# Kernel tuning notes

Measured on AMD Instinct MI355X. Metric: run time of the kernel, lower is better.

Reference implementation:

```python
import jax, jax.numpy as jnp
import numpy as np

B, S, H, NH, T = 4, 512, 512, 8, 3
DH = H // NH
DTS = H // T  # 170, per-timescale encoder width
EPS = 1e-5

def _ln(x, g, b):
    m = jnp.mean(x, axis=-1, keepdims=True)
    v = jnp.mean((x - m) ** 2, axis=-1, keepdims=True)
    return (x - m) * jax.lax.rsqrt(v + EPS) * g + b

def _gelu(x):
    return jax.nn.gelu(x, approximate=False)

def _mha(x, qkv_W, qkv_b, out_W, out_b, mask):
    # x: [B,S,H]; qkv_W: [H,3H]; mask: [B,S,S] float additive or None
    qkv = x @ qkv_W + qkv_b
    q, k, v = jnp.split(qkv, 3, axis=-1)
    q = q.reshape(B, S, NH, DH)
    k = k.reshape(B, S, NH, DH)
    v = v.reshape(B, S, NH, DH)
    scores = jnp.einsum('bqhd,bkhd->bhqk', q, k) / jnp.sqrt(jnp.float32(DH))
    if mask is not None:
        scores = scores + mask[:, None, :, :]
    attn = jax.nn.softmax(scores, axis=-1)
    o = jnp.einsum('bhqk,bkhd->bqhd', attn, v).reshape(B, S, H)
    return o @ out_W + out_b

def setup_inputs() -> dict:
    key = jax.random.key(0)
    ks = jax.random.split(key, 32)
    r = lambda i, shape, s=0.02: (jax.random.normal(ks[i], shape, dtype=jnp.float32) * s)
    inp = {}
    inp['x'] = jax.random.normal(ks[0], (B, S, H), dtype=jnp.float32)
    inp['timestamps'] = jax.random.uniform(ks[1], (B, S), dtype=jnp.float32) * 1e6
    # per-timescale encoders (stacked over T)
    inp['enc_W'] = r(2, (T, 2, DTS), 0.5)
    inp['enc_b'] = jnp.zeros((T, DTS), jnp.float32)
    inp['enc_ln_g'] = jnp.ones((T, DTS), jnp.float32)
    inp['enc_ln_b'] = jnp.zeros((T, DTS), jnp.float32)
    # per-timescale MHA
    inp['qkv_W'] = r(3, (T, H, 3 * H))
    inp['qkv_b'] = jnp.zeros((T, 3 * H), jnp.float32)
    inp['attn_out_W'] = r(4, (T, H, H))
    inp['attn_out_b'] = jnp.zeros((T, H), jnp.float32)
    # time mixer
    inp['mixer_W1'] = r(5, (T * H, H))
    inp['mixer_b1'] = jnp.zeros((H,), jnp.float32)
    inp['mixer_ln_g'] = jnp.ones((H,), jnp.float32)
    inp['mixer_ln_b'] = jnp.zeros((H,), jnp.float32)
    inp['mixer_W2'] = r(6, (H, T))
    inp['mixer_b2'] = jnp.zeros((T,), jnp.float32)
    # transformer encoder layer (post-norm, gelu, ffn=4H)
    inp['el_qkv_W'] = r(7, (H, 3 * H))
    inp['el_qkv_b'] = jnp.zeros((3 * H,), jnp.float32)
    inp['el_out_W'] = r(8, (H, H))
    inp['el_out_b'] = jnp.zeros((H,), jnp.float32)
    inp['el_ln1_g'] = jnp.ones((H,), jnp.float32)
    inp['el_ln1_b'] = jnp.zeros((H,), jnp.float32)
    inp['el_ff_W1'] = r(9, (H, 4 * H))
    inp['el_ff_b1'] = jnp.zeros((4 * H,), jnp.float32)
    inp['el_ff_W2'] = r(10, (4 * H, H))
    inp['el_ff_b2'] = jnp.zeros((H,), jnp.float32)
    inp['el_ln2_g'] = jnp.ones((H,), jnp.float32)
    inp['el_ln2_b'] = jnp.zeros((H,), jnp.float32)
    # output projection
    inp['op_W'] = r(11, (H, H))
    inp['op_b'] = jnp.zeros((H,), jnp.float32)
    inp['op_ln_g'] = jnp.ones((H,), jnp.float32)
    inp['op_ln_b'] = jnp.zeros((H,), jnp.float32)
    return inp

def reference(x, timestamps, enc_W, enc_b, enc_ln_g, enc_ln_b, qkv_W, qkv_b, attn_out_W, attn_out_b,
              mixer_W1, mixer_b1, mixer_ln_g, mixer_ln_b, mixer_W2, mixer_b2,
              el_qkv_W, el_qkv_b, el_out_W, el_out_b, el_ln1_g, el_ln1_b,
              el_ff_W1, el_ff_b1, el_ff_W2, el_ff_b2, el_ln2_g, el_ln2_b,
              op_W, op_b, op_ln_g, op_ln_b):
    # pairwise time features [B,S,S]
    time_diff = timestamps[:, :, None] - timestamps[:, None, :]
    direction = jnp.sign(time_diff)
    magnitude = jnp.log1p(jnp.abs(time_diff) / 3600.0)
    outs = []
    for i in range(T):
        mag = magnitude / (10.0 ** i)
        tf = jnp.stack([direction, mag], axis=-1)            # [B,S,S,2]
        e = tf @ enc_W[i] + enc_b[i]                          # [B,S,S,DTS]
        e = _gelu(_ln(e, enc_ln_g[i], enc_ln_b[i]))
        mask = jnp.mean(e, axis=-1)                           # [B,S,S] additive attn mask
        outs.append(_mha(x, qkv_W[i], qkv_b[i], attn_out_W[i], attn_out_b[i], mask))
    combined = jnp.concatenate(outs, axis=-1)                 # [B,S,T*H]
    m = _gelu(_ln(combined @ mixer_W1 + mixer_b1, mixer_ln_g, mixer_ln_b))
    mix = jax.nn.softmax(m @ mixer_W2 + mixer_b2, axis=-1)    # [B,S,T]
    weighted = sum(mix[..., i:i + 1] * outs[i] for i in range(T))
    # post-norm transformer encoder layer
    sa = _mha(weighted, el_qkv_W, el_qkv_b, el_out_W, el_out_b, None)
    h1 = _ln(weighted + sa, el_ln1_g, el_ln1_b)
    ff = _gelu(h1 @ el_ff_W1 + el_ff_b1) @ el_ff_W2 + el_ff_b2
    h2 = _ln(h1 + ff, el_ln2_g, el_ln2_b)
    out = _ln(h2 @ op_W + op_b, op_ln_g, op_ln_b)
    return out
```

## Files before the change

kernel.cpp:

```cpp
#include <hip/hip_runtime.h>
#include <hip/hip_bf16.h>
#include <math.h>

#define Bq 4
#define Sq 512
#define Hq 512
#define NHq 8
#define Tq 3
#define DTSq 170
#define BSq 2048
#define ENCSTRIDE 520
#define NLUT 2048
#define MAGMAXf 5.6304994f

typedef float f32x4 __attribute__((ext_vector_type(4)));
typedef __bf16 bf16x4 __attribute__((ext_vector_type(4)));
typedef __bf16 bf16x8 __attribute__((ext_vector_type(8)));

__device__ __forceinline__ float gelu_f(float x){
  return 0.5f * x * (1.0f + erff(x * 0.70710678118654752f));
}

__device__ __forceinline__ void gload16(const void* g, void* l){
  __builtin_amdgcn_global_load_lds((const __attribute__((address_space(1))) void*)g,
                                   (__attribute__((address_space(3))) void*)l, 16, 0, 0);
}

__device__ __forceinline__ float waveReduceSum(float v){
  #pragma unroll
  for (int off = 32; off > 0; off >>= 1) v += __shfl_xor(v, off);
  return v;
}

__device__ __forceinline__ float blockReduce(float v, float* red){
  int tid = threadIdx.x;
  __syncthreads();
  red[tid] = v; __syncthreads();
  for (int s = 128; s > 0; s >>= 1){
    if (tid < s) red[tid] += red[tid + s];
    __syncthreads();
  }
  return red[0];
}

__global__ __launch_bounds__(256) void enc_prep(const float* __restrict__ encW,
                                                const float* __restrict__ encB,
                                                float* __restrict__ out){
  int t = blockIdx.x, tid = threadIdx.x;
  __shared__ float red[256];
  const float* W0 = encW + t * 2 * DTSq;
  const float* W1 = W0 + DTSq;
  const float* Bv = encB + t * DTSq;
  float w0 = (tid < DTSq) ? W0[tid] : 0.f;
  float w1 = (tid < DTSq) ? W1[tid] : 0.f;
  float bv = (tid < DTSq) ? Bv[tid] : 0.f;
  const float invD = 1.0f / (float)DTSq;
  float m0 = blockReduce(w0, red) * invD;
  float m1 = blockReduce(w1, red) * invD;
  float mb = blockReduce(bv, red) * invD;
  float c0 = (tid < DTSq) ? (w0 - m0) : 0.f;
  float c1 = (tid < DTSq) ? (w1 - m1) : 0.f;
  float cb = (tid < DTSq) ? (bv - mb) : 0.f;
  float* op = out + t * ENCSTRIDE;
  if (tid < DTSq){
    op[tid] = c0; op[DTSq + tid] = c1; op[2 * DTSq + tid] = cb;
  }
  float pa = blockReduce(c0 * c0, red) * invD;
  float pb = blockReduce(c1 * c1, red) * invD;
  float pc = blockReduce(c0 * c1, red) * invD;
  float pd = blockReduce(c0 * cb, red) * invD;
  float pe = blockReduce(c1 * cb, red) * invD;
  float pf = blockReduce(cb * cb, red) * invD;
  if (tid == 0){
    op[3 * DTSq + 0] = pa; op[3 * DTSq + 1] = pb; op[3 * DTSq + 2] = pc;
    op[3 * DTSq + 3] = pd; op[3 * DTSq + 4] = pe; op[3 * DTSq + 5] = pf;
  }
}

__global__ __launch_bounds__(256) void mask_lut_build(const float* __restrict__ enc,
                                                      const float* __restrict__ g,
                                                      const float* __restrict__ be,
                                                      float* __restrict__ lut){
  int td = blockIdx.x;
  int t = td / 3, dsel = td % 3;
  float d = (float)(dsel - 1);
  __shared__ float sw0[DTSq], sw1[DTSq], sbc[DTSq], sg[DTSq], sbe[DTSq];
  const float* ep = enc + t * ENCSTRIDE;
  for (int c = threadIdx.x; c < DTSq; c += 256){
    sw0[c] = ep[c]; sw1[c] = ep[DTSq + c]; sbc[c] = ep[2 * DTSq + c];
    sg[c] = g[t * DTSq + c]; sbe[c] = be[t * DTSq + c];
  }
  __syncthreads();
  float A  = ep[3 * DTSq + 0], Bs = ep[3 * DTSq + 1], Cs = ep[3 * DTSq + 2];
  float Ds = ep[3 * DTSq + 3], Es = ep[3 * DTSq + 4], Fs = ep[3 * DTSq + 5];
  int e = blockIdx.y * 256 + threadIdx.x;
  float tscale = (t == 0) ? 1.f : ((t == 1) ? 0.1f : 0.01f);
  float m = (MAGMAXf / (float)(NLUT - 1)) * (float)e * tscale;
  float var = fabsf(d) * A + m * m * Bs + Fs + 2.f * (d * m * Cs + d * Ds + m * Es);
  float rs = rsqrtf(var + 1e-5f);
  float sum = 0.f;
  for (int c = 0; c < DTSq; ++c){
    float ee = fmaf(m, sw1[c], fmaf(d, sw0[c], sbc[c]));
    float n = fmaf(ee * rs, sg[c], sbe[c]);
    sum += n * 0.5f * (1.0f + erff(n * 0.70710678118654752f));
  }
  lut[td * NLUT + e] = sum * (1.0f / (float)DTSq);
}

__global__ __launch_bounds__(256) void mask_fill(const float* __restrict__ ts,
                                                 const float* __restrict__ lut,
                                                 __bf16* __restrict__ maskbuf){
  int bi = blockIdx.x;
  int b = bi >> 9, i = bi & 511;
  float tsi = ts[bi];
  for (int j0 = 0; j0 < Sq; j0 += 256){
    int j = j0 + threadIdx.x;
    float dt = tsi - ts[(b << 9) + j];
    int dsel = (dt > 0.f) ? 2 : ((dt < 0.f) ? 0 : 1);
    float mag = log1pf(fabsf(dt) * (1.0f / 3600.0f));
    float u = mag * ((float)(NLUT - 1) / MAGMAXf);
    int i0 = (int)u; if (i0 > NLUT - 2) i0 = NLUT - 2;
    float f = u - (float)i0;
    #pragma unroll
    for (int t = 0; t < Tq; ++t){
      const float* lp = lut + (t * 3 + dsel) * NLUT + i0;
      float v = lp[0] + f * (lp[1] - lp[0]);
      maskbuf[(((size_t)(t * Bq + b) * Sq + i) * Sq) + j] = (__bf16)v;
    }
  }
}

struct CvtEnt { const float* W; __bf16* WT; int ldw, ldt, ntn, start; };
struct CvtArgs { CvtEnt e[12]; };

__global__ __launch_bounds__(256) void cvt_wT_all(CvtArgs a){
  int bid = blockIdx.x;
  int i = 0;
  #pragma unroll
  for (int k = 1; k < 12; ++k) if (bid >= a.e[k].start) i = k;
  const float* W = a.e[i].W;
  __bf16* WT = a.e[i].WT;
  int ldw = a.e[i].ldw, ldt = a.e[i].ldt;
  int local = bid - a.e[i].start;
  int tn = local % a.e[i].ntn, tk = local / a.e[i].ntn;
  int n0 = tn * 64, k0 = tk * 64;
  __shared__ float T[64][65];
  int tid = threadIdx.x;
  #pragma unroll
  for (int q = 0; q < 16; ++q){
    int lin = q * 256 + tid;
    int r = lin >> 6, c = lin & 63;
    T[r][c] = W[(size_t)(k0 + r) * ldw + n0 + c];
  }
  __syncthreads();
  #pragma unroll
  for (int q = 0; q < 16; ++q){
    int lin = q * 256 + tid;
    int n = lin >> 6, k = lin & 63;
    WT[(size_t)(n0 + n) * ldt + k0 + k] = (__bf16)T[k][n];
  }
}

__global__ __launch_bounds__(256) void cvt_bf(const float* __restrict__ in,
                                              __bf16* __restrict__ out, int n){
  int idx = (blockIdx.x * 256 + threadIdx.x) * 4;
  if (idx < n){
    float4 v = *(const float4*)&in[idx];
    bf16x4 r; r[0]=(__bf16)v.x; r[1]=(__bf16)v.y; r[2]=(__bf16)v.z; r[3]=(__bf16)v.w;
    *(bf16x4*)&out[idx] = r;
  }
}

template<int BM>
__global__ __launch_bounds__(256) void gemm_pipe(
    const __bf16* __restrict__ A, int lda, size_t sAz,
    const __bf16* __restrict__ BT, int ldb, size_t sBz,
    const float* __restrict__ bias, int sBiasz,
    float* __restrict__ C32, __bf16* __restrict__ C16, int ldc, size_t sCz,
    int K, int act)
{
  constexpr int MF = BM / 32;
  constexpr int ABYTES = BM * 128;
  constexpr int BBYTES = 64 * 128;
  __shared__ __bf16 lds[(2 * (ABYTES + BBYTES)) / 2];
  int tid = threadIdx.x;

  int gx = gridDim.x, nwg = gx * gridDim.y;
  int lin = blockIdx.x + gx * blockIdx.y;
  int q8 = nwg >> 3;
  int swz = (lin & 7) * q8 + (lin >> 3);
  int bx = swz % gx, by = swz / gx;

  int z = blockIdx.z;
  A  += (size_t)z * sAz;
  BT += (size_t)z * sBz;
  const float* bz = bias ? bias + (size_t)z * sBiasz : nullptr;
  size_t cbase = (size_t)z * sCz;
  int brow = by * BM, bcol = bx * 64;

  int lane = tid & 63, w = tid >> 6;
  int wr = (w >> 1) * (BM / 2), wc = (w & 1) * 32;
  int lr = lane & 15, lg = lane >> 4;

  f32x4 acc[MF][2];
  #pragma unroll
  for (int m = 0; m < MF; ++m)
    #pragma unroll
    for (int n = 0; n < 2; ++n) acc[m][n] = (f32x4){0.f, 0.f, 0.f, 0.f};

  char* lbase = (char*)lds;

  auto stage = [&](int buf, int ko){
    char* ab = lbase + buf * (ABYTES + BBYTES);
    #pragma unroll
    for (int qq = 0; qq < BM / 32; ++qq){
      int byte = (qq * 256 + tid) * 16;
      int row = byte >> 7, col8 = byte & 127;
      int src = col8 ^ ((row & 7) << 4);
      gload16(&A[(size_t)(brow + row) * lda + ko + (src >> 1)], ab + byte);
    }
    char* bb = ab + ABYTES;
    #pragma unroll
    for (int qq = 0; qq < 2; ++qq){
      int byte = (qq * 256 + tid) * 16;
      int row = byte >> 7, col8 = byte & 127;
      int src = col8 ^ ((row & 7) << 4);
      gload16(&BT[(size_t)(bcol + row) * ldb + ko + (src >> 1)], bb + byte);
    }
  };

  stage(0, 0);
  int nk = K >> 6;
  for (int kt = 0; kt < nk; ++kt){
    int cur = kt & 1;
    if (kt + 1 < nk){
      stage(cur ^ 1, (kt + 1) << 6);
      if constexpr (BM == 64) asm volatile("s_waitcnt vmcnt(4)" ::: "memory");
      else                    asm volatile("s_waitcnt vmcnt(6)" ::: "memory");
    } else {
      asm volatile("s_waitcnt vmcnt(0)" ::: "memory");
    }
    __builtin_amdgcn_s_barrier();
    __builtin_amdgcn_sched_barrier(0);
    char* ab = lbase + cur * (ABYTES + BBYTES);
    char* bb = ab + ABYTES;
    #pragma unroll
    for (int s = 0; s < 2; ++s){
      bf16x8 af[MF], bfr[2];
      #pragma unroll
      for (int m = 0; m < MF; ++m){
        int row = wr + m * 16 + lr;
        int col8 = (s * 64 + lg * 16) ^ ((row & 7) << 4);
        af[m] = *(const bf16x8*)(ab + row * 128 + col8);
      }
      #pragma unroll
      for (int n = 0; n < 2; ++n){
        int row = wc + n * 16 + lr;
        int col8 = (s * 64 + lg * 16) ^ ((row & 7) << 4);
        bfr[n] = *(const bf16x8*)(bb + row * 128 + col8);
      }
      #pragma unroll
      for (int m = 0; m < MF; ++m)
        #pragma unroll
        for (int n = 0; n < 2; ++n)
          acc[m][n] = __builtin_amdgcn_mfma_f32_16x16x32_bf16(af[m], bfr[n], acc[m][n], 0, 0, 0);
    }
    asm volatile("" ::: "memory");
    __builtin_amdgcn_s_barrier();
  }

  #pragma unroll
  for (int m = 0; m < MF; ++m){
    #pragma unroll
    for (int n = 0; n < 2; ++n){
      int col = bcol + wc + n * 16 + lr;
      float bv = bz ? bz[col] : 0.f;
      #pragma unroll
      for (int j = 0; j < 4; ++j){
        int row = brow + wr + m * 16 + lg * 4 + j;
        float v = acc[m][n][j] + bv;
        if (act) v = gelu_f(v);
        size_t idx = cbase + (size_t)row * ldc + col;
        if (C32) C32[idx] = v;
        if (C16) C16[idx] = (__bf16)v;
      }
    }
  }
}

template<bool HM>
__global__ __launch_bounds__(256) void flash_attn(
    const __bf16* __restrict__ qkv, size_t sQz,
    const __bf16* __restrict__ vt,  size_t sVz,
    const __bf16* __restrict__ mask, size_t sMz,
    __bf16* __restrict__ ctx, size_t sCz)
{
  int t = blockIdx.z;
  qkv += (size_t)t * sQz;
  vt  += (size_t)t * sVz;
  ctx += (size_t)t * sCz;
  const __bf16* mk = HM ? mask + (size_t)t * sMz : nullptr;

  int lin = blockIdx.x + (blockIdx.y << 3);
  int swz = (lin & 7) * 32 + (lin >> 3);
  int io = (swz & 7) * 64;
  int bh = swz >> 3;
  int b = bh >> 3, h = bh & 7;

  constexpr int KB = 64 * 128;
  __shared__ __bf16 lds[(2 * 2 * KB) / 2];
  __shared__ __bf16 Ps[4][16][72];
  int tid = threadIdx.x, lane = tid & 63, w = tid >> 6;
  int lr = lane & 15, lg = lane >> 4;

  const __bf16* qrow = &qkv[(size_t)(b * Sq + io + w * 16 + lr) * 1536 + h * 64];
  bf16x8 q0 = *(const bf16x8*)&qrow[lg * 8];
  bf16x8 q1 = *(const bf16x8*)&qrow[32 + lg * 8];

  char* lb = (char*)lds;
  auto stage = [&](int buf, int jo){
    char* kb = lb + buf * (2 * KB);
    #pragma unroll
    for (int qq = 0; qq < 2; ++qq){
      int byte = (qq * 256 + tid) * 16;
      int row = byte >> 7, col8 = byte & 127;
      int src = col8 ^ ((row & 7) << 4);
      gload16(&qkv[(size_t)(b * Sq + jo + row) * 1536 + 512 + h * 64 + (src >> 1)], kb + byte);
    }
    char* vb = kb + KB;
    #pragma unroll
    for (int qq = 0; qq < 2; ++qq){
      int byte = (qq * 256 + tid) * 16;
      int row = byte >> 7, col8 = byte & 127;
      int src = col8 ^ ((row & 7) << 4);
      gload16(&vt[((size_t)bh * 64 + row) * Sq + jo + (src >> 1)], vb + byte);
    }
  };

  f32x4 o[4];
  #pragma unroll
  for (int n = 0; n < 4; ++n) o[n] = (f32x4){0.f, 0.f, 0.f, 0.f};
  float mrow[4] = {-1e30f, -1e30f, -1e30f, -1e30f};
  float lrow[4] = {0.f, 0.f, 0.f, 0.f};

  stage(0, 0);
  #pragma unroll
  for (int kt = 0; kt < 8; ++kt){
    int cur = kt & 1;
    int jo = kt << 6;

    float mv[4][4];
    if (HM){
      #pragma unroll
      for (int n = 0; n < 4; ++n)
        #pragma unroll
        for (int reg = 0; reg < 4; ++reg)
          mv[n][reg] = (float)mk[((size_t)(b * Sq + io + w * 16 + lg * 4 + reg)) * Sq + jo + n * 16 + lr];
    }

    if (kt + 1 < 8){
      stage(cur ^ 1, (kt + 1) << 6);
      if (HM) asm volatile("s_waitcnt vmcnt(20)" ::: "memory");
      else    asm volatile("s_waitcnt vmcnt(4)"  ::: "memory");
    } else {
      asm volatile("s_waitcnt vmcnt(0)" ::: "memory");
    }
    __builtin_amdgcn_s_barrier();
    __builtin_amdgcn_sched_barrier(0);

    char* kb = lb + cur * (2 * KB);
    char* vb = kb + KB;

    f32x4 s4[4];
    #pragma unroll
    for (int n = 0; n < 4; ++n) s4[n] = (f32x4){0.f, 0.f, 0.f, 0.f};
    __builtin_amdgcn_s_setprio(1);
    #pragma unroll
    for (int s = 0; s < 2; ++s){
      bf16x8 aq = s ? q1 : q0;
      #pragma unroll
      for (int n = 0; n < 4; ++n){
        int row = n * 16 + lr;
        int colb = (s * 64 + lg * 16) ^ ((row & 7) << 4);
        bf16x8 bk = *(const bf16x8*)(kb + row * 128 + colb);
        s4[n] = __builtin_amdgcn_mfma_f32_16x16x32_bf16(aq, bk, s4[n], 0, 0, 0);
      }
    }
    __builtin_amdgcn_s_setprio(0);

    float sv[4][4];
    #pragma unroll
    for (int n = 0; n < 4; ++n)
      #pragma unroll
      for (int reg = 0; reg < 4; ++reg)
        sv[n][reg] = s4[n][reg] * 0.125f + (HM ? mv[n][reg] : 0.f);

    #pragma unroll
    for (int reg = 0; reg < 4; ++reg){
      float pmax = fmaxf(fmaxf(sv[0][reg], sv[1][reg]), fmaxf(sv[2][reg], sv[3][reg]));
      #pragma unroll
      for (int off = 1; off < 16; off <<= 1) pmax = fmaxf(pmax, __shfl_xor(pmax, off));
      if (pmax > mrow[reg] + 8.0f){
        float corr = __expf(mrow[reg] - pmax);
        mrow[reg] = pmax;
        lrow[reg] *= corr;
        #pragma unroll
        for (int n = 0; n < 4; ++n) o[n][reg] *= corr;
      }
      float rs = 0.f;
      #pragma unroll
      for (int n = 0; n < 4; ++n){
        float p = __expf(sv[n][reg] - mrow[reg]);
        sv[n][reg] = p;
        rs += p;
      }
      #pragma unroll
      for (int off = 1; off < 16; off <<= 1) rs += __shfl_xor(rs, off);
      lrow[reg] += rs;
    }

    #pragma unroll
    for (int n = 0; n < 4; ++n)
      #pragma unroll
      for (int reg = 0; reg < 4; ++reg)
        Ps[w][lg * 4 + reg][n * 16 + lr] = (__bf16)sv[n][reg];
    __builtin_amdgcn_s_setprio(1);
    #pragma unroll
    for (int s = 0; s < 2; ++s){
      bf16x8 ap = *(const bf16x8*)&Ps[w][lr][s * 32 + lg * 8];
      #pragma unroll
      for (int n = 0; n < 4; ++n){
        int row = n * 16 + lr;
        int colb = (s * 64 + lg * 16) ^ ((row & 7) << 4);
        bf16x8 bv = *(const bf16x8*)(vb + row * 128 + colb);
        o[n] = __builtin_amdgcn_mfma_f32_16x16x32_bf16(ap, bv, o[n], 0, 0, 0);
      }
    }
    __builtin_amdgcn_s_setprio(0);

    asm volatile("" ::: "memory");
    __builtin_amdgcn_s_barrier();
  }

  #pragma unroll
  for (int reg = 0; reg < 4; ++reg){
    float inv = 1.0f / lrow[reg];
    int row = b * Sq + io + w * 16 + lg * 4 + reg;
    #pragma unroll
    for (int n = 0; n < 4; ++n)
      ctx[(size_t)row * Hq + h * 64 + n * 16 + lr] = (__bf16)(o[n][reg] * inv);
  }
}

__global__ __launch_bounds__(256) void ln_rows(const float* __restrict__ in,
                                               const float* __restrict__ res,
                                               const float* __restrict__ g,
                                               const float* __restrict__ bb,
                                               float* __restrict__ out32,
                                               __bf16* __restrict__ out16,
                                               int do_gelu){
  int row = blockIdx.x * 4 + (threadIdx.x >> 6);
  int lane = threadIdx.x & 63;
  const float* ir = in + (size_t)row * Hq;
  const float* rr = res ? res + (size_t)row * Hq : nullptr;
  float x[8]; float s = 0.f, sq = 0.f;
  #pragma unroll
  for (int k = 0; k < 8; ++k){
    int c = lane + 64 * k;
    float v = ir[c];
    if (rr) v += rr[c];
    x[k] = v; s += v; sq += v * v;
  }
  s = waveReduceSum(s); sq = waveReduceSum(sq);
  float mean = s * (1.0f / Hq);
  float var = fmaxf(sq * (1.0f / Hq) - mean * mean, 0.f);
  float rstd = rsqrtf(var + 1e-5f);
  #pragma unroll
  for (int k = 0; k < 8; ++k){
    int c = lane + 64 * k;
    float y = (x[k] - mean) * rstd * g[c] + bb[c];
    if (do_gelu) y = gelu_f(y);
    if (out32) out32[(size_t)row * Hq + c] = y;
    if (out16) out16[(size_t)row * Hq + c] = (__bf16)y;
  }
}

__global__ __launch_bounds__(256) void ln_mixer_weighted(const float* __restrict__ in,
                                                         const float* __restrict__ g,
                                                         const float* __restrict__ bb,
                                                         const float* __restrict__ W2,
                                                         const float* __restrict__ b2,
                                                         const __bf16* __restrict__ comb,
                                                         float* __restrict__ out32,
                                                         __bf16* __restrict__ out16){
  int row = blockIdx.x * 4 + (threadIdx.x >> 6);
  int lane = threadIdx.x & 63;
  const float* ir = in + (size_t)row * Hq;
  float x[8]; float s = 0.f, sq = 0.f;
  #pragma unroll
  for (int k = 0; k < 8; ++k){
    int c = lane + 64 * k;
    float v = ir[c];
    x[k] = v; s += v; sq += v * v;
  }
  s = waveReduceSum(s); sq = waveReduceSum(sq);
  float mean = s * (1.0f / Hq);
  float var = fmaxf(sq * (1.0f / Hq) - mean * mean, 0.f);
  float rstd = rsqrtf(var + 1e-5f);
  float a0 = 0.f, a1 = 0.f, a2 = 0.f;
  #pragma unroll
  for (int k = 0; k < 8; ++k){
    int c = lane + 64 * k;
    float y = gelu_f((x[k] - mean) * rstd * g[c] + bb[c]);
    const float* wv = W2 + c * 3;
    a0 = fmaf(y, wv[0], a0); a1 = fmaf(y, wv[1], a1); a2 = fmaf(y, wv[2], a2);
  }
  a0 = waveReduceSum(a0) + b2[0];
  a1 = waveReduceSum(a1) + b2[1];
  a2 = waveReduceSum(a2) + b2[2];
  float mx = fmaxf(a0, fmaxf(a1, a2));
  float e0 = __expf(a0 - mx), e1 = __expf(a1 - mx), e2 = __expf(a2 - mx);
  float inv = 1.0f / (e0 + e1 + e2);
  float m0 = e0 * inv, m1 = e1 * inv, m2 = e2 * inv;
  const __bf16* cr = comb + (size_t)row * 1536;
  #pragma unroll
  for (int k = 0; k < 8; ++k){
    int c = lane + 64 * k;
    float v = m0 * (float)cr[c] + m1 * (float)cr[512 + c] + m2 * (float)cr[1024 + c];
    out32[(size_t)row * Hq + c] = v;
    out16[(size_t)row * Hq + c] = (__bf16)v;
  }
}

__global__ __launch_bounds__(256) void transpose_v(const __bf16* __restrict__ qkv, size_t sQz,
                                                   __bf16* __restrict__ vt, size_t sVz){
  int t = blockIdx.z;
  qkv += (size_t)t * sQz;
  vt  += (size_t)t * sVz;
  int bh = blockIdx.y, b = bh >> 3, h = bh & 7;
  int so = blockIdx.x * 64;
  __shared__ __bf16 T[64][72];
  int tid = threadIdx.x;
  #pragma unroll
  for (int q = 0; q < 16; ++q){
    int lin = q * 256 + tid;
    int r = lin >> 6, c = lin & 63;
    T[r][c] = qkv[(size_t)(b * Sq + so + r) * 1536 + 1024 + h * 64 + c];
  }
  __syncthreads();
  #pragma unroll
  for (int q = 0; q < 16; ++q){
    int lin = q * 256 + tid;
    int d = lin >> 6, s = lin & 63;
    vt[((size_t)bh * 64 + d) * Sq + so + s] = T[s][d];
  }
}

extern "C" void kernel_launch(void* const* d_in, const int* in_sizes, int n_in,
                              void* d_out, int out_size, void* d_ws, size_t ws_size,
                              hipStream_t stream){
  const float* x         = (const float*)d_in[0];
  const float* ts        = (const float*)d_in[1];
  const float* enc_W     = (const float*)d_in[2];
  const float* enc_b     = (const float*)d_in[3];
  const float* enc_ln_g  = (const float*)d_in[4];
  const float* enc_ln_b  = (const float*)d_in[5];
  const float* qkv_W     = (const float*)d_in[6];
  const float* qkv_b     = (const float*)d_in[7];
  const float* aout_W    = (const float*)d_in[8];
  const float* aout_b    = (const float*)d_in[9];
  const float* mx_W1     = (const float*)d_in[10];
  const float* mx_b1     = (const float*)d_in[11];
  const float* mx_ln_g   = (const float*)d_in[12];
  const float* mx_ln_b   = (const float*)d_in[13];
  const float* mx_W2     = (const float*)d_in[14];
  const float* mx_b2     = (const float*)d_in[15];
  const float* el_qkv_W  = (const float*)d_in[16];
  const float* el_qkv_b  = (const float*)d_in[17];
  const float* el_out_W  = (const float*)d_in[18];
  const float* el_out_b  = (const float*)d_in[19];
  const float* el_ln1_g  = (const float*)d_in[20];
  const float* el_ln1_b  = (const float*)d_in[21];
  const float* el_ff_W1  = (const float*)d_in[22];
  const float* el_ff_b1  = (const float*)d_in[23];
  const float* el_ff_W2  = (const float*)d_in[24];
  const float* el_ff_b2  = (const float*)d_in[25];
  const float* el_ln2_g  = (const float*)d_in[26];
  const float* el_ln2_b  = (const float*)d_in[27];
  const float* op_W      = (const float*)d_in[28];
  const float* op_b      = (const float*)d_in[29];
  const float* op_ln_g   = (const float*)d_in[30];
  const float* op_ln_b   = (const float*)d_in[31];

  float* ws = (float*)d_ws;
  size_t o = 0;
  __bf16* MASKBb = (__bf16*)(ws + o); o += 1572864;
  __bf16* XB     = (__bf16*)(ws + o); o += 524288;
  __bf16* qkvT   = (__bf16*)(ws + o); o += 1179648;
  __bf16* aoutT  = (__bf16*)(ws + o); o += 393216;
  __bf16* mx1T   = (__bf16*)(ws + o); o += 393216;
  __bf16* elqkvT = (__bf16*)(ws + o); o += 393216;
  __bf16* eloutT = (__bf16*)(ws + o); o += 131072;
  __bf16* ff1T   = (__bf16*)(ws + o); o += 524288;
  __bf16* ff2T   = (__bf16*)(ws + o); o += 524288;
  __bf16* opT    = (__bf16*)(ws + o); o += 131072;
  __bf16* QKVb   = (__bf16*)(ws + o); o += 4718592;
  __bf16* VTb    = (__bf16*)(ws + o); o += 1572864;
  __bf16* FFBb   = (__bf16*)(ws + o); o += 2097152;
  __bf16* CTXb   = (__bf16*)(ws + o); o += 1572864;
  __bf16* COMBb  = (__bf16*)(ws + o); o += 1572864;
  float*  MBUF   = ws + o;            o += 1048576;
  float*  WEI    = ws + o;            o += 1048576;
  __bf16* WEIb   = (__bf16*)(ws + o); o += 524288;
  float*  SA     = ws + o;            o += 1048576;
  float*  H1     = ws + o;            o += 1048576;
  __bf16* H1b    = (__bf16*)(ws + o); o += 524288;
  float*  H2     = ws + o;            o += 1048576;
  __bf16* H2b    = (__bf16*)(ws + o); o += 524288;
  float*  ENC    = ws + o;            o += 1600;
  float*  LUTB   = ws + o;            o += 9 * NLUT;
  float*  OPO    = MBUF;

  cvt_bf<<<1024, 256, 0, stream>>>(x, XB, BSq * Hq);
  {
    CvtArgs ca;
    for (int t = 0; t < 3; ++t)
      ca.e[t] = {qkv_W + (size_t)t * 512 * 1536, qkvT + (size_t)t * 1536 * 512, 1536, 512, 24, 192 * t};
    for (int t = 0; t < 3; ++t)
      ca.e[3 + t] = {aout_W + (size_t)t * 512 * 512, aoutT + (size_t)t * 512 * 512, 512, 512, 8, 576 + 64 * t};
    ca.e[6]  = {mx_W1,    mx1T,   512,  1536, 8,  768};
    ca.e[7]  = {el_qkv_W, elqkvT, 1536, 512,  24, 960};
    ca.e[8]  = {el_out_W, eloutT, 512,  512,  8,  1152};
    ca.e[9]  = {el_ff_W1, ff1T,   2048, 512,  32, 1216};
    ca.e[10] = {el_ff_W2, ff2T,   512,  2048, 8,  1472};
    ca.e[11] = {op_W,     opT,    512,  512,  8,  1728};
    cvt_wT_all<<<1792, 256, 0, stream>>>(ca);
  }

  enc_prep<<<Tq, 256, 0, stream>>>(enc_W, enc_b, ENC);
  mask_lut_build<<<dim3(9, NLUT / 256), 256, 0, stream>>>(ENC, enc_ln_g, enc_ln_b, LUTB);
  mask_fill<<<BSq, 256, 0, stream>>>(ts, LUTB, MASKBb);

  gemm_pipe<128><<<dim3(24, 16, 3), 256, 0, stream>>>(XB, 512, 0, qkvT, 512, (size_t)1536 * 512,
      qkv_b, 1536, nullptr, QKVb, 1536, (size_t)2048 * 1536, 512, 0);
  transpose_v<<<dim3(8, 32, 3), 256, 0, stream>>>(QKVb, (size_t)2048 * 1536, VTb, (size_t)32 * 64 * 512);
  flash_attn<true><<<dim3(8, 32, 3), 256, 0, stream>>>(QKVb, (size_t)2048 * 1536,
      VTb, (size_t)32 * 64 * 512, MASKBb, (size_t)4 * 512 * 512, CTXb, (size_t)2048 * 512);
  gemm_pipe<64><<<dim3(8, 32, 3), 256, 0, stream>>>(CTXb, 512, (size_t)2048 * 512, aoutT, 512, (size_t)512 * 512,
      aout_b, 512, nullptr, COMBb, 1536, 512, 512, 0);

  gemm_pipe<64><<<dim3(8, 32, 1), 256, 0, stream>>>(COMBb, 1536, 0, mx1T, 1536, 0,
      mx_b1, 0, MBUF, nullptr, 512, 0, 1536, 0);
  ln_mixer_weighted<<<512, 256, 0, stream>>>(MBUF, mx_ln_g, mx_ln_b, mx_W2, mx_b2, COMBb, WEI, WEIb);

  gemm_pipe<128><<<dim3(24, 16, 1), 256, 0, stream>>>(WEIb, 512, 0, elqkvT, 512, 0,
      el_qkv_b, 0, nullptr, QKVb, 1536, 0, 512, 0);
  transpose_v<<<dim3(8, 32, 1), 256, 0, stream>>>(QKVb, 0, VTb, 0);
  flash_attn<false><<<dim3(8, 32, 1), 256, 0, stream>>>(QKVb, 0, VTb, 0, nullptr, 0, CTXb, 0);
  gemm_pipe<64><<<dim3(8, 32, 1), 256, 0, stream>>>(CTXb, 512, 0, eloutT, 512, 0,
      el_out_b, 0, SA, nullptr, 512, 0, 512, 0);
  ln_rows<<<512, 256, 0, stream>>>(WEI, SA, el_ln1_g, el_ln1_b, H1, H1b, 0);
  gemm_pipe<128><<<dim3(32, 16, 1), 256, 0, stream>>>(H1b, 512, 0, ff1T, 512, 0,
      el_ff_b1, 0, nullptr, FFBb, 2048, 0, 512, 1);
  gemm_pipe<64><<<dim3(8, 32, 1), 256, 0, stream>>>(FFBb, 2048, 0, ff2T, 2048, 0,
      el_ff_b2, 0, SA, nullptr, 512, 0, 2048, 0);
  ln_rows<<<512, 256, 0, stream>>>(H1, SA, el_ln2_g, el_ln2_b, H2, H2b, 0);

  gemm_pipe<64><<<dim3(8, 32, 1), 256, 0, stream>>>(H2b, 512, 0, opT, 512, 0,
      op_b, 0, OPO, nullptr, 512, 0, 512, 0);
  ln_rows<<<512, 256, 0, stream>>>(OPO, nullptr, op_ln_g, op_ln_b, (float*)d_out, nullptr, 0);
}
```

Baseline: 217.0 us.

## Stage attention mask via async LDS loads, shrink N-tile for narrow GEMMs, fuse enc prep

Flash attention now brings each mask tile into LDS with async global_load_lds in the same double-buffered pipeline as K/V. Before, every mask element was read with scattered scalar global loads. The mask buffer is then reused as the P staging area, which removes the separate Ps array. The narrow N=512 GEMMs get a BN template parameter and run with 64x32 tiles, which doubles their grid for better CU occupancy. enc_prep is merged into mask_lut_build, so one launch and one global round-trip go away, at the cost of recomputing the statistics in every block.

```diff
diff --git a/kernel.cpp b/kernel.cpp
--- a/kernel.cpp
+++ b/kernel.cpp
@@ -9,7 +9,6 @@
 #define Tq 3
 #define DTSq 170
 #define BSq 2048
-#define ENCSTRIDE 520
 #define NLUT 2048
 #define MAGMAXf 5.6304994f
 
@@ -43,11 +42,18 @@
   return red[0];
 }
 
-__global__ __launch_bounds__(256) void enc_prep(const float* __restrict__ encW,
-                                                const float* __restrict__ encB,
-                                                float* __restrict__ out){
-  int t = blockIdx.x, tid = threadIdx.x;
+__global__ __launch_bounds__(256) void mask_lut_build(const float* __restrict__ encW,
+                                                      const float* __restrict__ encB,
+                                                      const float* __restrict__ g,
+                                                      const float* __restrict__ be,
+                                                      float* __restrict__ lut){
+  int td = blockIdx.x;
+  int t = td / 3, dsel = td % 3;
+  float d = (float)(dsel - 1);
   __shared__ float red[256];
+  __shared__ float sw0[DTSq], sw1[DTSq], sbc[DTSq], sg[DTSq], sbe[DTSq];
+  __shared__ float sS[6];
+  int tid = threadIdx.x;
   const float* W0 = encW + t * 2 * DTSq;
   const float* W1 = W0 + DTSq;
   const float* Bv = encB + t * DTSq;
@@ -61,9 +67,9 @@
   float c0 = (tid < DTSq) ? (w0 - m0) : 0.f;
   float c1 = (tid < DTSq) ? (w1 - m1) : 0.f;
   float cb = (tid < DTSq) ? (bv - mb) : 0.f;
-  float* op = out + t * ENCSTRIDE;
   if (tid < DTSq){
-    op[tid] = c0; op[DTSq + tid] = c1; op[2 * DTSq + tid] = cb;
+    sw0[tid] = c0; sw1[tid] = c1; sbc[tid] = cb;
+    sg[tid] = g[t * DTSq + tid]; sbe[tid] = be[t * DTSq + tid];
   }
   float pa = blockReduce(c0 * c0, red) * invD;
   float pb = blockReduce(c1 * c1, red) * invD;
@@ -71,29 +77,10 @@
   float pd = blockReduce(c0 * cb, red) * invD;
   float pe = blockReduce(c1 * cb, red) * invD;
   float pf = blockReduce(cb * cb, red) * invD;
-  if (tid == 0){
-    op[3 * DTSq + 0] = pa; op[3 * DTSq + 1] = pb; op[3 * DTSq + 2] = pc;
-    op[3 * DTSq + 3] = pd; op[3 * DTSq + 4] = pe; op[3 * DTSq + 5] = pf;
-  }
-}
-
-__global__ __launch_bounds__(256) void mask_lut_build(const float* __restrict__ enc,
-                                                      const float* __restrict__ g,
-                                                      const float* __restrict__ be,
-                                                      float* __restrict__ lut){
-  int td = blockIdx.x;
-  int t = td / 3, dsel = td % 3;
-  float d = (float)(dsel - 1);
-  __shared__ float sw0[DTSq], sw1[DTSq], sbc[DTSq], sg[DTSq], sbe[DTSq];
-  const float* ep = enc + t * ENCSTRIDE;
-  for (int c = threadIdx.x; c < DTSq; c += 256){
-    sw0[c] = ep[c]; sw1[c] = ep[DTSq + c]; sbc[c] = ep[2 * DTSq + c];
-    sg[c] = g[t * DTSq + c]; sbe[c] = be[t * DTSq + c];
-  }
+  if (tid == 0){ sS[0]=pa; sS[1]=pb; sS[2]=pc; sS[3]=pd; sS[4]=pe; sS[5]=pf; }
   __syncthreads();
-  float A  = ep[3 * DTSq + 0], Bs = ep[3 * DTSq + 1], Cs = ep[3 * DTSq + 2];
-  float Ds = ep[3 * DTSq + 3], Es = ep[3 * DTSq + 4], Fs = ep[3 * DTSq + 5];
-  int e = blockIdx.y * 256 + threadIdx.x;
+  float A = sS[0], Bs = sS[1], Cs = sS[2], Ds = sS[3], Es = sS[4], Fs = sS[5];
+  int e = blockIdx.y * 256 + tid;
   float tscale = (t == 0) ? 1.f : ((t == 1) ? 0.1f : 0.01f);
   float m = (MAGMAXf / (float)(NLUT - 1)) * (float)e * tscale;
   float var = fabsf(d) * A + m * m * Bs + Fs + 2.f * (d * m * Cs + d * Ds + m * Es);
@@ -171,7 +158,7 @@
   }
 }
 
-template<int BM>
+template<int BM, int BN>
 __global__ __launch_bounds__(256) void gemm_pipe(
     const __bf16* __restrict__ A, int lda, size_t sAz,
     const __bf16* __restrict__ BT, int ldb, size_t sBz,
@@ -180,8 +167,10 @@
     int K, int act)
 {
   constexpr int MF = BM / 32;
+  constexpr int NF = BN / 32;
+  constexpr int LOADS = MF + NF;
   constexpr int ABYTES = BM * 128;
-  constexpr int BBYTES = 64 * 128;
+  constexpr int BBYTES = BN * 128;
   __shared__ __bf16 lds[(2 * (ABYTES + BBYTES)) / 2];
   int tid = threadIdx.x;
 
@@ -196,24 +185,24 @@
   BT += (size_t)z * sBz;
   const float* bz = bias ? bias + (size_t)z * sBiasz : nullptr;
   size_t cbase = (size_t)z * sCz;
-  int brow = by * BM, bcol = bx * 64;
+  int brow = by * BM, bcol = bx * BN;
 
   int lane = tid & 63, w = tid >> 6;
-  int wr = (w >> 1) * (BM / 2), wc = (w & 1) * 32;
+  int wr = (w >> 1) * (BM / 2), wc = (w & 1) * (BN / 2);
   int lr = lane & 15, lg = lane >> 4;
 
-  f32x4 acc[MF][2];
+  f32x4 acc[MF][NF];
   #pragma unroll
   for (int m = 0; m < MF; ++m)
     #pragma unroll
-    for (int n = 0; n < 2; ++n) acc[m][n] = (f32x4){0.f, 0.f, 0.f, 0.f};
+    for (int n = 0; n < NF; ++n) acc[m][n] = (f32x4){0.f, 0.f, 0.f, 0.f};
 
   char* lbase = (char*)lds;
 
   auto stage = [&](int buf, int ko){
     char* ab = lbase + buf * (ABYTES + BBYTES);
     #pragma unroll
-    for (int qq = 0; qq < BM / 32; ++qq){
+    for (int qq = 0; qq < MF; ++qq){
       int byte = (qq * 256 + tid) * 16;
       int row = byte >> 7, col8 = byte & 127;
       int src = col8 ^ ((row & 7) << 4);
@@ -221,7 +210,7 @@
     }
     char* bb = ab + ABYTES;
     #pragma unroll
-    for (int qq = 0; qq < 2; ++qq){
+    for (int qq = 0; qq < NF; ++qq){
       int byte = (qq * 256 + tid) * 16;
       int row = byte >> 7, col8 = byte & 127;
       int src = col8 ^ ((row & 7) << 4);
@@ -235,8 +224,9 @@
     int cur = kt & 1;
     if (kt + 1 < nk){
       stage(cur ^ 1, (kt + 1) << 6);
-      if constexpr (BM == 64) asm volatile("s_waitcnt vmcnt(4)" ::: "memory");
-      else                    asm volatile("s_waitcnt vmcnt(6)" ::: "memory");
+      if constexpr (LOADS == 3)      asm volatile("s_waitcnt vmcnt(3)" ::: "memory");
+      else if constexpr (LOADS == 4) asm volatile("s_waitcnt vmcnt(4)" ::: "memory");
+      else                           asm volatile("s_waitcnt vmcnt(6)" ::: "memory");
     } else {
       asm volatile("s_waitcnt vmcnt(0)" ::: "memory");
     }
@@ -246,7 +236,7 @@
     char* bb = ab + ABYTES;
     #pragma unroll
     for (int s = 0; s < 2; ++s){
-      bf16x8 af[MF], bfr[2];
+      bf16x8 af[MF], bfr[NF];
       #pragma unroll
       for (int m = 0; m < MF; ++m){
         int row = wr + m * 16 + lr;
@@ -254,7 +244,7 @@
         af[m] = *(const bf16x8*)(ab + row * 128 + col8);
       }
       #pragma unroll
-      for (int n = 0; n < 2; ++n){
+      for (int n = 0; n < NF; ++n){
         int row = wc + n * 16 + lr;
         int col8 = (s * 64 + lg * 16) ^ ((row & 7) << 4);
         bfr[n] = *(const bf16x8*)(bb + row * 128 + col8);
@@ -262,7 +252,7 @@
       #pragma unroll
       for (int m = 0; m < MF; ++m)
         #pragma unroll
-        for (int n = 0; n < 2; ++n)
+        for (int n = 0; n < NF; ++n)
           acc[m][n] = __builtin_amdgcn_mfma_f32_16x16x32_bf16(af[m], bfr[n], acc[m][n], 0, 0, 0);
     }
     asm volatile("" ::: "memory");
@@ -272,7 +262,7 @@
   #pragma unroll
   for (int m = 0; m < MF; ++m){
     #pragma unroll
-    for (int n = 0; n < 2; ++n){
+    for (int n = 0; n < NF; ++n){
       int col = bcol + wc + n * 16 + lr;
       float bv = bz ? bz[col] : 0.f;
       #pragma unroll
@@ -307,9 +297,10 @@
   int bh = swz >> 3;
   int b = bh >> 3, h = bh & 7;
 
-  constexpr int KB = 64 * 128;
-  __shared__ __bf16 lds[(2 * 2 * KB) / 2];
-  __shared__ __bf16 Ps[4][16][72];
+  constexpr int TB = 8192;
+  constexpr int BUFB = HM ? 3 * TB : 2 * TB;
+  __shared__ char lds[2 * BUFB + (HM ? 0 : TB)];
+  char* lb = lds;
   int tid = threadIdx.x, lane = tid & 63, w = tid >> 6;
   int lr = lane & 15, lg = lane >> 4;
 
@@ -317,23 +308,32 @@
   bf16x8 q0 = *(const bf16x8*)&qrow[lg * 8];
   bf16x8 q1 = *(const bf16x8*)&qrow[32 + lg * 8];
 
-  char* lb = (char*)lds;
   auto stage = [&](int buf, int jo){
-    char* kb = lb + buf * (2 * KB);
+    char* kb = lb + buf * BUFB;
     #pragma unroll
     for (int qq = 0; qq < 2; ++qq){
       int byte = (qq * 256 + tid) * 16;
-      int row = byte >> 7, col8 = byte & 127;
-      int src = col8 ^ ((row & 7) << 4);
+      int row = byte >> 7;
+      int src = (byte & 127) ^ ((row & 7) << 4);
       gload16(&qkv[(size_t)(b * Sq + jo + row) * 1536 + 512 + h * 64 + (src >> 1)], kb + byte);
     }
-    char* vb = kb + KB;
+    char* vb = kb + TB;
     #pragma unroll
     for (int qq = 0; qq < 2; ++qq){
       int byte = (qq * 256 + tid) * 16;
-      int row = byte >> 7, col8 = byte & 127;
-      int src = col8 ^ ((row & 7) << 4);
+      int row = byte >> 7;
+      int src = (byte & 127) ^ ((row & 7) << 4);
       gload16(&vt[((size_t)bh * 64 + row) * Sq + jo + (src >> 1)], vb + byte);
+    }
+    if constexpr (HM){
+      char* mb = vb + TB;
+      #pragma unroll
+      for (int qq = 0; qq < 2; ++qq){
+        int byte = (qq * 256 + tid) * 16;
+        int row = byte >> 7;
+        int src = (byte & 127) ^ ((row & 7) << 4);
+        gload16(&mk[(size_t)(b * Sq + io + row) * Sq + jo + (src >> 1)], mb + byte);
+      }
     }
   };
 
@@ -347,29 +347,20 @@
   #pragma unroll
   for (int kt = 0; kt < 8; ++kt){
     int cur = kt & 1;
-    int jo = kt << 6;
-
-    float mv[4][4];
-    if (HM){
-      #pragma unroll
-      for (int n = 0; n < 4; ++n)
-        #pragma unroll
-        for (int reg = 0; reg < 4; ++reg)
-          mv[n][reg] = (float)mk[((size_t)(b * Sq + io + w * 16 + lg * 4 + reg)) * Sq + jo + n * 16 + lr];
-    }
 
     if (kt + 1 < 8){
       stage(cur ^ 1, (kt + 1) << 6);
-      if (HM) asm volatile("s_waitcnt vmcnt(20)" ::: "memory");
-      else    asm volatile("s_waitcnt vmcnt(4)"  ::: "memory");
+      if constexpr (HM) asm volatile("s_waitcnt vmcnt(6)" ::: "memory");
+      else              asm volatile("s_waitcnt vmcnt(4)" ::: "memory");
     } else {
       asm volatile("s_waitcnt vmcnt(0)" ::: "memory");
     }
     __builtin_amdgcn_s_barrier();
     __builtin_amdgcn_sched_barrier(0);
 
-    char* kb = lb + cur * (2 * KB);
-    char* vb = kb + KB;
+    char* kb = lb + cur * BUFB;
+    char* vb = kb + TB;
+    char* mb = HM ? vb + TB : lb + 2 * BUFB;
 
     f32x4 s4[4];
     #pragma unroll
@@ -390,10 +381,18 @@
 
     float sv[4][4];
     #pragma unroll
-    for (int n = 0; n < 4; ++n)
-      #pragma unroll
-      for (int reg = 0; reg < 4; ++reg)
-        sv[n][reg] = s4[n][reg] * 0.125f + (HM ? mv[n][reg] : 0.f);
+    for (int n = 0; n < 4; ++n){
+      #pragma unroll
+      for (int reg = 0; reg < 4; ++reg){
+        float v = s4[n][reg] * 0.125f;
+        if constexpr (HM){
+          int row = w * 16 + lg * 4 + reg;
+          int off = ((n * 16 + lr) * 2) ^ ((row & 7) << 4);
+          v += (float)*(const __bf16*)(mb + row * 128 + off);
+        }
+        sv[n][reg] = v;
+      }
+    }
 
     #pragma unroll
     for (int reg = 0; reg < 4; ++reg){
@@ -422,12 +421,17 @@
     #pragma unroll
     for (int n = 0; n < 4; ++n)
       #pragma unroll
-      for (int reg = 0; reg < 4; ++reg)
-        Ps[w][lg * 4 + reg][n * 16 + lr] = (__bf16)sv[n][reg];
+      for (int reg = 0; reg < 4; ++reg){
+        int row = w * 16 + lg * 4 + reg;
+        int off = ((n * 16 + lr) * 2) ^ ((row & 7) << 4);
+        *(__bf16*)(mb + row * 128 + off) = (__bf16)sv[n][reg];
+      }
     __builtin_amdgcn_s_setprio(1);
     #pragma unroll
     for (int s = 0; s < 2; ++s){
-      bf16x8 ap = *(const bf16x8*)&Ps[w][lr][s * 32 + lg * 8];
+      int arow = w * 16 + lr;
+      int acol = (s * 64 + lg * 16) ^ ((arow & 7) << 4);
+      bf16x8 ap = *(const bf16x8*)(mb + arow * 128 + acol);
       #pragma unroll
       for (int n = 0; n < 4; ++n){
         int row = n * 16 + lr;
@@ -617,7 +621,6 @@
   __bf16* H1b    = (__bf16*)(ws + o); o += 524288;
   float*  H2     = ws + o;            o += 1048576;
   __bf16* H2b    = (__bf16*)(ws + o); o += 524288;
-  float*  ENC    = ws + o;            o += 1600;
   float*  LUTB   = ws + o;            o += 9 * NLUT;
   float*  OPO    = MBUF;
 
@@ -637,36 +640,35 @@
     cvt_wT_all<<<1792, 256, 0, stream>>>(ca);
   }
 
-  enc_prep<<<Tq, 256, 0, stream>>>(enc_W, enc_b, ENC);
-  mask_lut_build<<<dim3(9, NLUT / 256), 256, 0, stream>>>(ENC, enc_ln_g, enc_ln_b, LUTB);
+  mask_lut_build<<<dim3(9, NLUT / 256), 256, 0, stream>>>(enc_W, enc_b, enc_ln_g, enc_ln_b, LUTB);
   mask_fill<<<BSq, 256, 0, stream>>>(ts, LUTB, MASKBb);
 
-  gemm_pipe<128><<<dim3(24, 16, 3), 256, 0, stream>>>(XB, 512, 0, qkvT, 512, (size_t)1536 * 512,
+  gemm_pipe<128,64><<<dim3(24, 16, 3), 256, 0, stream>>>(XB, 512, 0, qkvT, 512, (size_t)1536 * 512,
       qkv_b, 1536, nullptr, QKVb, 1536, (size_t)2048 * 1536, 512, 0);
   transpose_v<<<dim3(8, 32, 3), 256, 0, stream>>>(QKVb, (size_t)2048 * 1536, VTb, (size_t)32 * 64 * 512);
   flash_attn<true><<<dim3(8, 32, 3), 256, 0, stream>>>(QKVb, (size_t)2048 * 1536,
       VTb, (size_t)32 * 64 * 512, MASKBb, (size_t)4 * 512 * 512, CTXb, (size_t)2048 * 512);
-  gemm_pipe<64><<<dim3(8, 32, 3), 256, 0, stream>>>(CTXb, 512, (size_t)2048 * 512, aoutT, 512, (size_t)512 * 512,
+  gemm_pipe<64,32><<<dim3(16, 32, 3), 256, 0, stream>>>(CTXb, 512, (size_t)2048 * 512, aoutT, 512, (size_t)512 * 512,
       aout_b, 512, nullptr, COMBb, 1536, 512, 512, 0);
 
-  gemm_pipe<64><<<dim3(8, 32, 1), 256, 0, stream>>>(COMBb, 1536, 0, mx1T, 1536, 0,
+  gemm_pipe<64,32><<<dim3(16, 32, 1), 256, 0, stream>>>(COMBb, 1536, 0, mx1T, 1536, 0,
       mx_b1, 0, MBUF, nullptr, 512, 0, 1536, 0);
   ln_mixer_weighted<<<512, 256, 0, stream>>>(MBUF, mx_ln_g, mx_ln_b, mx_W2, mx_b2, COMBb, WEI, WEIb);
 
-  gemm_pipe<128><<<dim3(24, 16, 1), 256, 0, stream>>>(WEIb, 512, 0, elqkvT, 512, 0,
+  gemm_pipe<128,64><<<dim3(24, 16, 1), 256, 0, stream>>>(WEIb, 512, 0, elqkvT, 512, 0,
       el_qkv_b, 0, nullptr, QKVb, 1536, 0, 512, 0);
   transpose_v<<<dim3(8, 32, 1), 256, 0, stream>>>(QKVb, 0, VTb, 0);
   flash_attn<false><<<dim3(8, 32, 1), 256, 0, stream>>>(QKVb, 0, VTb, 0, nullptr, 0, CTXb, 0);
-  gemm_pipe<64><<<dim3(8, 32, 1), 256, 0, stream>>>(CTXb, 512, 0, eloutT, 512, 0,
+  gemm_pipe<64,32><<<dim3(16, 32, 1), 256, 0, stream>>>(CTXb, 512, 0, eloutT, 512, 0,
       el_out_b, 0, SA, nullptr, 512, 0, 512, 0);
   ln_rows<<<512, 256, 0, stream>>>(WEI, SA, el_ln1_g, el_ln1_b, H1, H1b, 0);
-  gemm_pipe<128><<<dim3(32, 16, 1), 256, 0, stream>>>(H1b, 512, 0, ff1T, 512, 0,
+  gemm_pipe<128,64><<<dim3(32, 16, 1), 256, 0, stream>>>(H1b, 512, 0, ff1T, 512, 0,
       el_ff_b1, 0, nullptr, FFBb, 2048, 0, 512, 1);
-  gemm_pipe<64><<<dim3(8, 32, 1), 256, 0, stream>>>(FFBb, 2048, 0, ff2T, 2048, 0,
+  gemm_pipe<64,32><<<dim3(16, 32, 1), 256, 0, stream>>>(FFBb, 2048, 0, ff2T, 2048, 0,
       el_ff_b2, 0, SA, nullptr, 512, 0, 2048, 0);
   ln_rows<<<512, 256, 0, stream>>>(H1, SA, el_ln2_g, el_ln2_b, H2, H2b, 0);
 
-  gemm_pipe<64><<<dim3(8, 32, 1), 256, 0, stream>>>(H2b, 512, 0, opT, 512, 0,
+  gemm_pipe<64,32><<<dim3(16, 32, 1), 256, 0, stream>>>(H2b, 512, 0, opT, 512, 0,
       op_b, 0, OPO, nullptr, 512, 0, 512, 0);
   ln_rows<<<512, 256, 0, stream>>>(OPO, nullptr, op_ln_g, op_ln_b, (float*)d_out, nullptr, 0);
 }
```

Measured after the change: 214.9 us. Within noise of the previous version (-1.0%).
